# Kernel tuning notes

Hardware: AMD Instinct MI355X
Metric: run time of the kernel (lower is better)

Reference implementation:

```python
import jax, jax.numpy as jnp
import numpy as np

N, E = 4096, 131072
IN, HID, OUT = 128, 128, 256
H4, C4 = 4, HID            # first/middle GAT: 4 heads of 128 -> concat 512
CAT = H4 * C4              # 512
NH, DK = 8, OUT // 8       # dense MHA
EPS_LN = 1e-5


def setup_inputs() -> dict:
    key = jax.random.key(0)
    ks = jax.random.split(key, 32)
    s = 0.05
    inp = {
        "x": jax.random.normal(ks[0], (N, IN), jnp.float32),
        "edge_index": jax.random.randint(ks[1], (2, E), 0, N, jnp.int64),
        # GAT layer 0: in=128, heads=4, out=128
        "W0": jax.random.normal(ks[2], (IN, H4 * C4)) * s,
        "as0": jax.random.normal(ks[3], (H4, C4)) * s,
        "ad0": jax.random.normal(ks[4], (H4, C4)) * s,
        "b0": jnp.zeros((H4 * C4,)),
        # GAT layer 1: in=512, heads=4, out=128
        "W1": jax.random.normal(ks[5], (CAT, H4 * C4)) * s,
        "as1": jax.random.normal(ks[6], (H4, C4)) * s,
        "ad1": jax.random.normal(ks[7], (H4, C4)) * s,
        "b1": jnp.zeros((H4 * C4,)),
        # GAT layer 2: in=512, heads=1, out=256
        "W2": jax.random.normal(ks[8], (CAT, OUT)) * s,
        "as2": jax.random.normal(ks[9], (1, OUT)) * s,
        "ad2": jax.random.normal(ks[10], (1, OUT)) * s,
        "b2": jnp.zeros((OUT,)),
        # LayerNorms
        "g0": jnp.ones((CAT,)), "be0": jnp.zeros((CAT,)),
        "g1": jnp.ones((CAT,)), "be1": jnp.zeros((CAT,)),
        "g2": jnp.ones((OUT,)), "be2": jnp.zeros((OUT,)),
        # dense MHA on output_dim=256
        "wq": jax.random.normal(ks[11], (OUT, OUT)) * s, "bq": jnp.zeros((OUT,)),
        "wk": jax.random.normal(ks[12], (OUT, OUT)) * s, "bk": jnp.zeros((OUT,)),
        "wv": jax.random.normal(ks[13], (OUT, OUT)) * s, "bv": jnp.zeros((OUT,)),
        "wo": jax.random.normal(ks[14], (OUT, OUT)) * s, "bo": jnp.zeros((OUT,)),
    }
    return inp


def _layer_norm(x, g, b):
    mu = x.mean(-1, keepdims=True)
    var = ((x - mu) ** 2).mean(-1, keepdims=True)
    return (x - mu) * jax.lax.rsqrt(var + EPS_LN) * g + b


def _gat(x, src, dst, W, a_src, a_dst, bias, heads, out_c):
    # PyG GATConv (concat=True, negative_slope=0.2, self-loops pre-added)
    n = x.shape[0]
    xl = (x @ W).reshape(n, heads, out_c)            # [N,H,C]
    al_s = (xl * a_src).sum(-1)                      # [N,H]
    al_d = (xl * a_dst).sum(-1)                      # [N,H]
    alpha = jax.nn.leaky_relu(al_s[src] + al_d[dst], 0.2)  # [Etot,H]
    m = jax.ops.segment_max(alpha, dst, num_segments=n)
    e = jnp.exp(alpha - m[dst])
    denom = jax.ops.segment_sum(e, dst, num_segments=n)
    w = e / (denom[dst] + 1e-16)                     # [Etot,H]
    msg = w[:, :, None] * xl[src]                    # [Etot,H,C]
    out = jax.ops.segment_sum(msg, dst, num_segments=n)
    return out.reshape(n, heads * out_c) + bias


def _mha(x, wq, bq, wk, bk, wv, bv, wo, bo):
    # x: [1,N,D], 8 heads
    B, S, D = x.shape
    def split(y):
        return y.reshape(B, S, NH, DK).transpose(0, 2, 1, 3)
    Q, K, V = split(x @ wq + bq), split(x @ wk + bk), split(x @ wv + bv)
    scores = jnp.einsum('bhqd,bhkd->bhqk', Q, K) / np.sqrt(DK)
    attn = jax.nn.softmax(scores, axis=-1)
    out = jnp.einsum('bhqk,bhkd->bhqd', attn, V)
    out = out.transpose(0, 2, 1, 3).reshape(B, S, D)
    return out @ wo + bo


def reference(x, edge_index, W0, as0, ad0, b0, W1, as1, ad1, b1, W2, as2, ad2, b2,
              g0, be0, g1, be1, g2, be2, wq, bq, wk, bk, wv, bv, wo, bo):
    n = x.shape[0]
    loops = jnp.arange(n, dtype=edge_index.dtype)
    src = jnp.concatenate([edge_index[0], loops])
    dst = jnp.concatenate([edge_index[1], loops])

    # layer 0: in=128 -> 512; residual None (128 != 512)
    h = jax.nn.elu(_gat(x, src, dst, W0, as0, ad0, b0, H4, C4))
    h = _layer_norm(h, g0, be0)

    # layer 1: 512 -> 512; residual applies
    res = h
    h = jax.nn.elu(_gat(h, src, dst, W1, as1, ad1, b1, H4, C4))
    h = _layer_norm(h, g1, be1)
    h = h + res

    # layer 2: 512 -> 256, 1 head
    h = _gat(h, src, dst, W2, as2, ad2, b2, 1, OUT)
    h = _layer_norm(h, g2, be2)

    # dense self-attention over all nodes as one sequence
    h = _mha(h[None], wq, bq, wk, bk, wv, bv, wo, bo)[0]
    return h
```

## Files before the change

kernel.cpp:

```cpp
#include <hip/hip_runtime.h>
#include <math.h>

typedef __attribute__((ext_vector_type(8))) short short8;
typedef __attribute__((ext_vector_type(4))) float float4v;

#define QS 0.2550354f

#if __has_builtin(__builtin_amdgcn_exp2f)
#define EXP2(x) __builtin_amdgcn_exp2f(x)
#else
#define EXP2(x) __expf((x)*0.6931471805599453f)
#endif

__device__ __forceinline__ float waveReduceSum(float v){
  #pragma unroll
  for(int o=32;o>0;o>>=1) v += __shfl_down(v,o,64);
  return v;
}

__device__ __forceinline__ unsigned short f2bf(float f){
  unsigned int u = __float_as_uint(f);
  return (unsigned short)((u + 0x7FFFu + ((u>>16)&1u)) >> 16);
}
__device__ __forceinline__ float bf2f(unsigned short u){
  return __uint_as_float(((unsigned int)u)<<16);
}

__global__ __launch_bounds__(256) void prep(const float* __restrict__ x, unsigned short* __restrict__ xb,
                     const float* __restrict__ W0, unsigned short* __restrict__ W0t,
                     const float* __restrict__ W1, unsigned short* __restrict__ W1t,
                     const float* __restrict__ W2, unsigned short* __restrict__ W2t,
                     const float* __restrict__ wq, const float* __restrict__ wk,
                     const float* __restrict__ wv, unsigned short* __restrict__ wqkvt,
                     const float* __restrict__ bq, const float* __restrict__ bk,
                     const float* __restrict__ bv, float* __restrict__ bqkv,
                     const float* __restrict__ wo, unsigned short* __restrict__ wot,
                     const float* __restrict__ as0, const float* __restrict__ ad0, unsigned short* __restrict__ S0,
                     const float* __restrict__ as1, const float* __restrict__ ad1, unsigned short* __restrict__ S1,
                     const float* __restrict__ as2, const float* __restrict__ ad2, unsigned short* __restrict__ S2,
                     const int* __restrict__ ei, int E, int Etot, int* __restrict__ hist){
  int b = blockIdx.x, t = threadIdx.x;
  if(b < 256){
    int i = (b*256 + t)*8;
    float4 u0 = *(const float4*)(x + i);
    float4 u1 = *(const float4*)(x + i + 4);
    short8 o;
    o[0]=(short)f2bf(u0.x); o[1]=(short)f2bf(u0.y); o[2]=(short)f2bf(u0.z); o[3]=(short)f2bf(u0.w);
    o[4]=(short)f2bf(u1.x); o[5]=(short)f2bf(u1.y); o[6]=(short)f2bf(u1.z); o[7]=(short)f2bf(u1.w);
    *(short8*)(xb + i) = o;
    return;
  }
  if(b == 256){ bqkv[t] = bq[t]*QS; bqkv[256+t] = bk[t]; bqkv[512+t] = bv[t]; return; }
  if(b < 433){
    __shared__ unsigned short tile[64][65];
    int tb = b - 257;
    const float* src; unsigned short* dst; int K,N,roff,local; float sc = 1.f;
    if(tb<16){src=W0;dst=W0t;K=128;N=512;local=tb;roff=0;}
    else if(tb<80){src=W1;dst=W1t;K=512;N=512;local=tb-16;roff=0;}
    else if(tb<112){src=W2;dst=W2t;K=512;N=256;local=tb-80;roff=0;}
    else if(tb<128){src=wq;dst=wqkvt;K=256;N=256;local=tb-112;roff=0;sc=QS;}
    else if(tb<144){src=wk;dst=wqkvt;K=256;N=256;local=tb-128;roff=256;}
    else if(tb<160){src=wv;dst=wqkvt;K=256;N=256;local=tb-144;roff=512;}
    else {src=wo;dst=wot;K=256;N=256;local=tb-160;roff=0;}
    int ntiles = N>>6;
    int k0 = (local/ntiles)*64, n0 = (local%ntiles)*64;
    int r4 = t>>4, c4 = (t&15)*4;
    #pragma unroll
    for(int it=0;it<4;it++){
      int row = r4 + it*16;
      float4 v = *(const float4*)(src + (size_t)(k0+row)*N + n0 + c4);
      tile[row][c4+0]=f2bf(v.x*sc);
      tile[row][c4+1]=f2bf(v.y*sc);
      tile[row][c4+2]=f2bf(v.z*sc);
      tile[row][c4+3]=f2bf(v.w*sc);
    }
    __syncthreads();
    int r8 = t>>3, c8 = (t&7)*8;
    #pragma unroll
    for(int it=0;it<2;it++){
      int n = r8 + it*32;
      short8 o;
      #pragma unroll
      for(int j=0;j<8;j++) o[j] = (short)tile[c8+j][n];
      *(short8*)(dst + (size_t)(n0+n+roff)*K + k0 + c8) = o;
    }
    return;
  }
  if(b >= 1585){
    int e = (b-1585)*256 + t;
    if(e < Etot){
      int d = (e<E) ? (ei[E+e]&4095) : (e-E);
      atomicAdd(&hist[d], 1);
    }
    return;
  }
  int bb = b - 433;
  const float *W,*as,*ad; unsigned short* S; int K,C,H,k;
  if(bb<128){W=W0;as=as0;ad=ad0;S=S0;K=128;C=128;H=4;k=bb;}
  else if(bb<640){W=W1;as=as1;ad=ad1;S=S1;K=512;C=128;H=4;k=bb-128;}
  else {W=W2;as=as2;ad=ad2;S=S2;K=512;C=256;H=1;k=bb-640;}
  int D = H*C;
  __shared__ float s1[4], s2[4];
  int lane=t&63, wid=t>>6;
  for(int h=0;h<H;h++){
    float ps=0.f, pd=0.f;
    for(int c=t;c<C;c+=256){
      float wv2 = W[k*D + h*C + c];
      ps += wv2*as[h*C+c];
      pd += wv2*ad[h*C+c];
    }
    ps = waveReduceSum(ps); pd = waveReduceSum(pd);
    if(lane==0){ s1[wid]=ps; s2[wid]=pd; }
    __syncthreads();
    if(t==0){
      float u=s1[0]+s1[1]+s1[2]+s1[3], v=s2[0]+s2[1]+s2[2]+s2[3];
      S[h*K+k]=f2bf(u); S[(4+h)*K+k]=f2bf(v);
    }
    __syncthreads();
  }
  if(t==0){
    for(int h=H;h<4;h++){ S[h*K+k]=0; S[(4+h)*K+k]=0; }
    for(int r=8;r<16;r++) S[r*K+k]=0;
  }
}

__global__ __launch_bounds__(256) void gemm_mfma(const unsigned short* __restrict__ A,
                                                 const unsigned short* __restrict__ Bt,
                                                 const float* __restrict__ bias,
                                                 float* __restrict__ C,
                                                 unsigned short* __restrict__ Cb,
                                                 unsigned short* __restrict__ VtT,
                                                 const unsigned short* __restrict__ Wsd,
                                                 float* __restrict__ als,
                                                 float* __restrict__ ald,
                                                 int M, int K, int N){
  int t = threadIdx.x, lane = t & 63, w = t >> 6;
  int m = lane & 15, g = lane >> 4;
  int bm = blockIdx.y * 64, bn = blockIdx.x * 64;

  __shared__ unsigned short As[2][64*72];
  __shared__ unsigned short Bs[2][64*72];

  int sr = t >> 3;
  int sc = (t & 7) * 8;
  const unsigned short* Ap = A  + (bm + sr)*K + sc;
  const unsigned short* Bp = Bt + (bn + sr)*K + sc;
  bool doC = (Wsd != nullptr) && (blockIdx.x == 0);

  float4v acc[4];
  #pragma unroll
  for(int nt=0;nt<4;nt++) acc[nt] = (float4v){0.f,0.f,0.f,0.f};
  float4v acc2 = (float4v){0.f,0.f,0.f,0.f};

  short8 a0 = *(const short8*)(Ap);
  short8 a1 = *(const short8*)(Ap + 32*K);
  short8 b0 = *(const short8*)(Bp);
  short8 b1 = *(const short8*)(Bp + 32*K);

  int buf = 0;
  for(int k0=0;k0<K;k0+=64){
    *(short8*)&As[buf][sr*72 + sc]      = a0;
    *(short8*)&As[buf][(sr+32)*72 + sc] = a1;
    *(short8*)&Bs[buf][sr*72 + sc]      = b0;
    *(short8*)&Bs[buf][(sr+32)*72 + sc] = b1;
    if(k0+64 < K){
      a0 = *(const short8*)(Ap + k0+64);
      a1 = *(const short8*)(Ap + 32*K + k0+64);
      b0 = *(const short8*)(Bp + k0+64);
      b1 = *(const short8*)(Bp + 32*K + k0+64);
    }
    __syncthreads();

    #pragma unroll
    for(int ks=0;ks<2;ks++){
      short8 aA = *(const short8*)&As[buf][(w*16 + m)*72 + ks*32 + g*8];
      #pragma unroll
      for(int nt=0;nt<4;nt++){
        short8 bB = *(const short8*)&Bs[buf][(nt*16 + m)*72 + ks*32 + g*8];
        acc[nt] = __builtin_amdgcn_mfma_f32_16x16x32_bf16(aA, bB, acc[nt], 0,0,0);
      }
      if(doC){
        short8 bW = *(const short8*)(Wsd + m*K + k0 + ks*32 + g*8);
        acc2 = __builtin_amdgcn_mfma_f32_16x16x32_bf16(aA, bW, acc2, 0,0,0);
      }
    }
    buf ^= 1;
  }

  if(VtT && bn >= 512){
    __syncthreads();
    unsigned short* T = &As[0][0];
    #pragma unroll
    for(int nt=0;nt<4;nt++){
      int col = bn + nt*16 + m;
      float bv = bias ? bias[col] : 0.f;
      unsigned int r0 = __float_as_uint(acc[nt][0]+bv) + 0x8000u;
      unsigned int r1 = __float_as_uint(acc[nt][1]+bv) + 0x8000u;
      unsigned int r2 = __float_as_uint(acc[nt][2]+bv) + 0x8000u;
      unsigned int r3 = __float_as_uint(acc[nt][3]+bv) + 0x8000u;
      uint2 pk;
      pk.x = __builtin_amdgcn_perm(r1, r0, 0x07060302u);
      pk.y = __builtin_amdgcn_perm(r3, r2, 0x07060302u);
      *(uint2*)&T[(nt*16 + m)*72 + w*16 + g*4] = pk;
    }
    __syncthreads();
    int d  = t >> 2;
    int qc = (t & 3) * 16;
    short8 v0 = *(const short8*)&T[d*72 + qc];
    short8 v1 = *(const short8*)&T[d*72 + qc + 8];
    unsigned short* dst = VtT + (size_t)(bn - 512 + d)*M + bm + qc;
    *(short8*)(dst)     = v0;
    *(short8*)(dst + 8) = v1;
    return;
  }

  #pragma unroll
  for(int nt=0;nt<4;nt++){
    int col = bn + nt*16 + m;
    float bv = bias ? bias[col] : 0.f;
    #pragma unroll
    for(int r=0;r<4;r++){
      int row = bm + w*16 + g*4 + r;
      float v = acc[nt][r] + bv;
      if(C)  C[row*N + col]  = v;
      if(Cb) Cb[row*N + col] = f2bf(v);
    }
  }
  if(doC){
    #pragma unroll
    for(int r=0;r<4;r++){
      int row = bm + w*16 + g*4 + r;
      if(m<4)      als[row*4 + m]     = acc2[r];
      else if(m<8) ald[row*4 + (m-4)] = acc2[r];
    }
  }
}

__global__ __launch_bounds__(1024) void csr_scan(const int* __restrict__ hist,
                                                 int* __restrict__ row_ptr,
                                                 int* __restrict__ wcnt, int N){
  __shared__ int sh[1024];
  int t = threadIdx.x;
  int base[4];
  int s = 0;
  #pragma unroll
  for(int i=0;i<4;i++){ base[i]=s; s += hist[t*4+i]; }
  sh[t] = s;
  __syncthreads();
  for(int off=1; off<1024; off<<=1){
    int x = (t>=off) ? sh[t-off] : 0;
    __syncthreads();
    sh[t] += x;
    __syncthreads();
  }
  int excl = (t==0) ? 0 : sh[t-1];
  #pragma unroll
  for(int i=0;i<4;i++){
    row_ptr[t*4+i] = excl + base[i];
    wcnt[t*4+i]    = excl + base[i];
  }
  if(t==1023) row_ptr[N] = excl + s;
}

__global__ void csr_scatter(const int* __restrict__ ei, int E, int Etot,
                            int* __restrict__ wcnt, int* __restrict__ col){
  int e = blockIdx.x*256 + threadIdx.x;
  if(e>=Etot) return;
  int s,d;
  if(e<E){ s=ei[e]&4095; d=ei[E+e]&4095; } else { s=d=e-E; }
  int pos = atomicAdd(&wcnt[d], 1);
  col[pos] = s;
}

#define CE 128
__global__ void gat_gather_ln(const int* __restrict__ rp,
                              const int* __restrict__ col,
                              const unsigned short* __restrict__ xlb,
                              const float* __restrict__ als,
                              const float* __restrict__ ald,
                              const float* __restrict__ bias,
                              const float* __restrict__ gw,
                              const float* __restrict__ be,
                              const float* __restrict__ res,
                              float* __restrict__ out,
                              unsigned short* __restrict__ outb,
                              int D, int logC, int do_elu){
  int n = blockIdx.x, t = threadIdx.x;
  int c0 = t*2;
  int h = c0 >> logC;
  int rowW = D >> 1;
  float4 advv = *(const float4*)(ald + n*4);
  int start = rp[n], end = rp[n+1];
  const unsigned int* xw = (const unsigned int*)xlb;

  __shared__ float pw[2][CE*4];
  __shared__ int offs[2][CE];

  float acc0=0.f, acc1=0.f, den=0.f;
  int nch = (end - start + CE - 1) / CE;

  {
    int cnt = min(CE, end-start);
    if(t < cnt){
      int s = col[start+t];
      offs[0][t] = s*rowW;
      float4 av = *(const float4*)(als + s*4);
      #pragma unroll
      for(int hh=0;hh<4;hh++){
        float a = ((const float*)&av)[hh] + ((const float*)&advv)[hh];
        a = a>0.f ? a : 0.2f*a;
        pw[0][t*4+hh] = __expf(a);
      }
    }
  }

  for(int c=0;c<nch;c++){
    __syncthreads();
    if(c+1 < nch){
      int base = start + (c+1)*CE;
      int cnt = min(CE, end-base);
      int b2 = (c+1)&1;
      if(t < cnt){
        int s = col[base+t];
        offs[b2][t] = s*rowW;
        float4 av = *(const float4*)(als + s*4);
        #pragma unroll
        for(int hh=0;hh<4;hh++){
          float a = ((const float*)&av)[hh] + ((const float*)&advv)[hh];
          a = a>0.f ? a : 0.2f*a;
          pw[b2][t*4+hh] = __expf(a);
        }
      }
    }
    int base = start + c*CE;
    int cnt = min(CE, end-base);
    int b = c&1;
    #pragma unroll 8
    for(int j=0;j<cnt;j++){
      float p = pw[b][j*4+h];
      unsigned int u = xw[offs[b][j] + t];
      acc0 += p * bf2f((unsigned short)(u & 0xffffu));
      acc1 += p * bf2f((unsigned short)(u >> 16));
      den += p;
    }
  }

  float inv_d = 1.f/(den + 1e-16f);
  float v0 = acc0*inv_d + bias[c0];
  float v1 = acc1*inv_d + bias[c0+1];
  if(do_elu){
    v0 = v0>0.f ? v0 : expm1f(v0);
    v1 = v1>0.f ? v1 : expm1f(v1);
  }
  __shared__ float sh[4];
  int lane=t&63, wid=t>>6, nw = blockDim.x>>6;
  float sum = waveReduceSum(v0+v1);
  if(lane==0) sh[wid]=sum;
  __syncthreads();
  float mean = 0.f;
  for(int i=0;i<nw;i++) mean += sh[i];
  mean /= (float)D;
  __syncthreads();
  float d0 = v0-mean, d1 = v1-mean;
  float vs = waveReduceSum(d0*d0 + d1*d1);
  if(lane==0) sh[wid]=vs;
  __syncthreads();
  float var = 0.f;
  for(int i=0;i<nw;i++) var += sh[i];
  var /= (float)D;
  float inv = rsqrtf(var + 1e-5f);
  float y0 = d0*inv*gw[c0]   + be[c0];
  float y1 = d1*inv*gw[c0+1] + be[c0+1];
  if(res){ float2 rv = *(const float2*)(res + n*D + c0); y0 += rv.x; y1 += rv.y; }
  if(out) *(float2*)(out + n*D + c0) = make_float2(y0, y1);
  if(outb) ((unsigned int*)outb)[n*rowW + t] =
      (unsigned int)f2bf(y0) | ((unsigned int)f2bf(y1) << 16);
}

#define KS 4
__global__ __launch_bounds__(256) void attention12(const unsigned short* __restrict__ QKV,
                                                   const unsigned short* __restrict__ Vt,
                                                   float* __restrict__ Op,
                                                   float* __restrict__ lp, int S){
  const int RS = 768;
  int qb = blockIdx.x * 64;
  int h  = blockIdx.y;
  int ks = blockIdx.z;
  int t  = threadIdx.x;
  int lane = t & 63, w = t >> 6;
  int m = lane & 15, g = lane >> 4;
  int m7 = m & 7;

  __shared__ unsigned short Ps[64*64];
  __shared__ unsigned short Vs[32*64];
  __shared__ unsigned short Ks[64*36];

  short8 aQ = *(const short8*)(QKV + (qb + w*16 + m)*RS + h*32 + g*8);

  float4v o0 = {0.f,0.f,0.f,0.f}, o1 = {0.f,0.f,0.f,0.f};
  float den = 0.f;

  int r8 = t>>3, c8 = t&7;
  int kr = t>>2, kc = (t&3)*8;
  int kA = ks*(S/KS), kB = kA + S/KS;

  short8 v  = *(const short8*)(Vt + (h*32 + r8)*S + kA + c8*8);
  short8 kv = *(const short8*)(QKV + (kA + kr)*RS + 256 + h*32 + kc);

  for(int kt=kA; kt<kB; kt+=64){
    __syncthreads();
    *(short8*)&Vs[r8*64 + ((c8 ^ (r8&7))<<3)] = v;
    *(short8*)&Ks[kr*36 + kc] = kv;
    if(kt+64 < kB){
      v  = *(const short8*)(Vt + (h*32 + r8)*S + kt+64 + c8*8);
      kv = *(const short8*)(QKV + (kt+64 + kr)*RS + 256 + h*32 + kc);
    }
    __syncthreads();

    #pragma unroll
    for(int nt=0;nt<4;nt++){
      short8 aK = *(const short8*)&Ks[(nt*16 + m)*36 + g*8];
      float4v acc = {0.f,0.f,0.f,0.f};
      acc = __builtin_amdgcn_mfma_f32_16x16x32_bf16(aK, aQ, acc, 0,0,0);
      float p0 = EXP2(acc[0]);
      float p1 = EXP2(acc[1]);
      float p2 = EXP2(acc[2]);
      float p3 = EXP2(acc[3]);
      den += (p0+p1)+(p2+p3);
      unsigned int r0 = __float_as_uint(p0) + 0x8000u;
      unsigned int r1 = __float_as_uint(p1) + 0x8000u;
      unsigned int r2 = __float_as_uint(p2) + 0x8000u;
      unsigned int r3 = __float_as_uint(p3) + 0x8000u;
      uint2 pk;
      pk.x = __builtin_amdgcn_perm(r1, r0, 0x07060302u);
      pk.y = __builtin_amdgcn_perm(r3, r2, 0x07060302u);
      *(uint2*)&Ps[(w*16 + m)*64 + (((2*nt + (g>>1)) ^ m7)<<3) + ((g&1)<<2)] = pk;
    }

    #pragma unroll
    for(int kh=0;kh<2;kh++){
      int swz = ((kh*4 + g) ^ m7) << 3;
      short8 aP  = *(const short8*)&Ps[(w*16 + m)*64 + swz];
      short8 bV0 = *(const short8*)&Vs[m*64       + swz];
      short8 bV1 = *(const short8*)&Vs[(16+m)*64  + swz];
      o0 = __builtin_amdgcn_mfma_f32_16x16x32_bf16(aP, bV0, o0, 0,0,0);
      o1 = __builtin_amdgcn_mfma_f32_16x16x32_bf16(aP, bV1, o1, 0,0,0);
    }
  }

  den += __shfl_xor(den, 16, 64);
  den += __shfl_xor(den, 32, 64);

  float* Ob = Op + (size_t)ks*S*256;
  #pragma unroll
  for(int r=0;r<4;r++){
    int q = qb + w*16 + g*4 + r;
    Ob[q*256 + h*32 + m]      = o0[r];
    Ob[q*256 + h*32 + 16 + m] = o1[r];
  }
  if(g==0){
    int q = qb + w*16 + m;
    lp[ks*S*8 + q*8 + h] = den;
  }
}

__global__ __launch_bounds__(256) void combine(const float* __restrict__ Op,
                                               const float* __restrict__ lp,
                                               unsigned short* __restrict__ aob, int S){
  int q = blockIdx.x, t = threadIdx.x;
  int h = t >> 5;
  float o = 0.f, l = 0.f;
  #pragma unroll
  for(int s=0;s<KS;s++) o += Op[(size_t)s*S*256 + q*256 + t];
  #pragma unroll
  for(int s=0;s<KS;s++) l += lp[s*S*8 + q*8 + h];
  aob[q*256 + t] = f2bf(o / l);
}

extern "C" void kernel_launch(void* const* d_in, const int* in_sizes, int n_in,
                              void* d_out, int out_size, void* d_ws, size_t ws_size,
                              hipStream_t stream) {
  const float* x   = (const float*)d_in[0];
  const int*   ei  = (const int*)d_in[1];
  const float* W0  = (const float*)d_in[2];
  const float* as0 = (const float*)d_in[3];
  const float* ad0 = (const float*)d_in[4];
  const float* b0  = (const float*)d_in[5];
  const float* W1  = (const float*)d_in[6];
  const float* as1 = (const float*)d_in[7];
  const float* ad1 = (const float*)d_in[8];
  const float* b1  = (const float*)d_in[9];
  const float* W2  = (const float*)d_in[10];
  const float* as2 = (const float*)d_in[11];
  const float* ad2 = (const float*)d_in[12];
  const float* b2  = (const float*)d_in[13];
  const float* g0  = (const float*)d_in[14];
  const float* be0 = (const float*)d_in[15];
  const float* g1  = (const float*)d_in[16];
  const float* be1 = (const float*)d_in[17];
  const float* g2  = (const float*)d_in[18];
  const float* be2 = (const float*)d_in[19];
  const float* wq  = (const float*)d_in[20];
  const float* bq  = (const float*)d_in[21];
  const float* wk  = (const float*)d_in[22];
  const float* bk  = (const float*)d_in[23];
  const float* wv  = (const float*)d_in[24];
  const float* bv  = (const float*)d_in[25];
  const float* wo  = (const float*)d_in[26];
  const float* bo  = (const float*)d_in[27];
  float* out = (float*)d_out;

  const int N = 4096;
  const int E = in_sizes[1] / 2;
  const int Etot = E + N;

  char* p = (char*)d_ws;
  auto alloc = [&](size_t bytes){ char* r = p; p += (bytes + 255) & ~(size_t)255; return r; };

  float* h0   = (float*)alloc(N*512*4);
  float* als  = (float*)alloc(N*4*4);
  float* ald  = (float*)alloc(N*4*4);
  unsigned short* xb   = (unsigned short*)alloc(N*128*2);
  unsigned short* xlb  = (unsigned short*)alloc(N*512*2);
  unsigned short* h0b  = (unsigned short*)alloc(N*512*2);
  unsigned short* h1b  = (unsigned short*)alloc(N*512*2);
  unsigned short* h2b  = (unsigned short*)alloc(N*256*2);
  unsigned short* QKVb = (unsigned short*)alloc((size_t)N*768*2);
  unsigned short* Vt   = (unsigned short*)alloc(256*N*2);
  unsigned short* aob  = (unsigned short*)alloc(N*256*2);
  unsigned short* W0t  = (unsigned short*)alloc(512*128*2);
  unsigned short* W1t  = (unsigned short*)alloc(512*512*2);
  unsigned short* W2t  = (unsigned short*)alloc(256*512*2);
  unsigned short* wqkvt= (unsigned short*)alloc(768*256*2);
  float* bqkv = (float*)alloc(768*4);
  unsigned short* wot  = (unsigned short*)alloc(256*256*2);
  unsigned short* Wsd0 = (unsigned short*)alloc(16*128*2);
  unsigned short* Wsd1 = (unsigned short*)alloc(16*512*2);
  unsigned short* Wsd2 = (unsigned short*)alloc(16*512*2);
  float* Op = (float*)alloc((size_t)KS*N*256*4);
  float* lp = (float*)alloc((size_t)KS*N*8*4);
  int* hist = (int*)alloc(N*4);
  int* wcnt = (int*)alloc(N*4);
  int* rp   = (int*)alloc((N+2)*4);
  int* col  = (int*)alloc(Etot*4);

  hipMemsetAsync(hist, 0, N*sizeof(int), stream);
  prep<<<1585 + (Etot+255)/256, 256, 0, stream>>>(x, xb, W0, W0t, W1, W1t, W2, W2t,
                                 wq, wk, wv, wqkvt, bq, bk, bv, bqkv, wo, wot,
                                 as0, ad0, Wsd0, as1, ad1, Wsd1, as2, ad2, Wsd2,
                                 ei, E, Etot, hist);

  csr_scan<<<1, 1024, 0, stream>>>(hist, rp, wcnt, N);
  csr_scatter<<<(Etot+255)/256, 256, 0, stream>>>(ei, E, Etot, wcnt, col);

  gemm_mfma<<<dim3(8, 64), 256, 0, stream>>>(xb, W0t, nullptr, nullptr, xlb, nullptr, Wsd0, als, ald, N, 128, 512);
  gat_gather_ln<<<N, 256, 0, stream>>>(rp, col, xlb, als, ald, b0, g0, be0,
                                       nullptr, h0, h0b, 512, 7, 1);

  gemm_mfma<<<dim3(8, 64), 256, 0, stream>>>(h0b, W1t, nullptr, nullptr, xlb, nullptr, Wsd1, als, ald, N, 512, 512);
  gat_gather_ln<<<N, 256, 0, stream>>>(rp, col, xlb, als, ald, b1, g1, be1,
                                       h0, nullptr, h1b, 512, 7, 1);

  gemm_mfma<<<dim3(4, 64), 256, 0, stream>>>(h1b, W2t, nullptr, nullptr, xlb, nullptr, Wsd2, als, ald, N, 512, 256);
  gat_gather_ln<<<N, 128, 0, stream>>>(rp, col, xlb, als, ald, b2, g2, be2,
                                       nullptr, nullptr, h2b, 256, 8, 0);

  gemm_mfma<<<dim3(12, 64), 256, 0, stream>>>(h2b, wqkvt, bqkv, nullptr, QKVb, Vt, nullptr, nullptr, nullptr, N, 256, 768);
  attention12<<<dim3(N/64, 8, KS), 256, 0, stream>>>(QKVb, Vt, Op, lp, N);
  combine<<<N, 256, 0, stream>>>(Op, lp, aob, N);
  gemm_mfma<<<dim3(4, 64), 256, 0, stream>>>(aob, wot, bo, out, nullptr, nullptr, nullptr, nullptr, nullptr, N, 256, 256);
}
```

Baseline: 268.1 us.

## Fold histogram into single-block scan, fuse edge scatter with first GEMM, halve attention split

The destination-degree histogram moves out of the prep kernel into the single-block CSR scan kernel, using shared-memory atomics, which removes the memset and the global atomics. The edge scatter that builds the CSR columns now runs as extra blocks of the layer-0 GEMM launch, so both share one launch and can run concurrently. The attention key-split factor drops from 4 to 2, which cuts partial-output traffic and combine work but leaves fewer attention blocks. The risk is that the single 1024-thread block walking all edges may be slower than the parallel global histogram.

```diff
diff --git a/kernel.cpp b/kernel.cpp
--- a/kernel.cpp
+++ b/kernel.cpp
@@ -17,7 +17,6 @@
   for(int o=32;o>0;o>>=1) v += __shfl_down(v,o,64);
   return v;
 }
-
 __device__ __forceinline__ unsigned short f2bf(float f){
   unsigned int u = __float_as_uint(f);
   return (unsigned short)((u + 0x7FFFu + ((u>>16)&1u)) >> 16);
@@ -37,8 +36,7 @@
                      const float* __restrict__ wo, unsigned short* __restrict__ wot,
                      const float* __restrict__ as0, const float* __restrict__ ad0, unsigned short* __restrict__ S0,
                      const float* __restrict__ as1, const float* __restrict__ ad1, unsigned short* __restrict__ S1,
-                     const float* __restrict__ as2, const float* __restrict__ ad2, unsigned short* __restrict__ S2,
-                     const int* __restrict__ ei, int E, int Etot, int* __restrict__ hist){
+                     const float* __restrict__ as2, const float* __restrict__ ad2, unsigned short* __restrict__ S2){
   int b = blockIdx.x, t = threadIdx.x;
   if(b < 256){
     int i = (b*256 + t)*8;
@@ -86,14 +84,6 @@
     }
     return;
   }
-  if(b >= 1585){
-    int e = (b-1585)*256 + t;
-    if(e < Etot){
-      int d = (e<E) ? (ei[E+e]&4095) : (e-E);
-      atomicAdd(&hist[d], 1);
-    }
-    return;
-  }
   int bb = b - 433;
   const float *W,*as,*ad; unsigned short* S; int K,C,H,k;
   if(bb<128){W=W0;as=as0;ad=ad0;S=S0;K=128;C=128;H=4;k=bb;}
@@ -124,28 +114,55 @@
   }
 }
 
-__global__ __launch_bounds__(256) void gemm_mfma(const unsigned short* __restrict__ A,
-                                                 const unsigned short* __restrict__ Bt,
-                                                 const float* __restrict__ bias,
-                                                 float* __restrict__ C,
-                                                 unsigned short* __restrict__ Cb,
-                                                 unsigned short* __restrict__ VtT,
-                                                 const unsigned short* __restrict__ Wsd,
-                                                 float* __restrict__ als,
-                                                 float* __restrict__ ald,
-                                                 int M, int K, int N){
+__global__ __launch_bounds__(1024) void csr_scan(const int* __restrict__ ei, int E, int Etot,
+                                                 int* __restrict__ rp, int* __restrict__ wcnt){
+  __shared__ int sh[1024];
+  __shared__ int lhist[4096];
+  int t = threadIdx.x;
+  #pragma unroll
+  for(int i=0;i<4;i++) lhist[t*4+i] = 0;
+  __syncthreads();
+  for(int e=t; e<Etot; e+=1024){
+    int d = (e<E) ? (ei[E+e]&4095) : (e-E);
+    atomicAdd(&lhist[d], 1);
+  }
+  __syncthreads();
+  int base[4]; int s=0;
+  #pragma unroll
+  for(int i=0;i<4;i++){ base[i]=s; s += lhist[t*4+i]; }
+  sh[t] = s;
+  __syncthreads();
+  for(int off=1; off<1024; off<<=1){
+    int x = (t>=off) ? sh[t-off] : 0;
+    __syncthreads();
+    sh[t] += x;
+    __syncthreads();
+  }
+  int excl = (t==0) ? 0 : sh[t-1];
+  #pragma unroll
+  for(int i=0;i<4;i++){
+    int v = excl + base[i];
+    rp[t*4+i] = v; wcnt[t*4+i] = v;
+  }
+  if(t==1023) rp[4096] = excl + s;
+}
+
+__device__ __forceinline__ void gemm_body(int bx, int by,
+                          const unsigned short* __restrict__ A, const unsigned short* __restrict__ Bt,
+                          const float* __restrict__ bias, float* __restrict__ C,
+                          unsigned short* __restrict__ Cb, unsigned short* __restrict__ VtT,
+                          const unsigned short* __restrict__ Wsd, float* __restrict__ als,
+                          float* __restrict__ ald, int M, int K, int N,
+                          unsigned short* As, unsigned short* Bs){
   int t = threadIdx.x, lane = t & 63, w = t >> 6;
   int m = lane & 15, g = lane >> 4;
-  int bm = blockIdx.y * 64, bn = blockIdx.x * 64;
-
-  __shared__ unsigned short As[2][64*72];
-  __shared__ unsigned short Bs[2][64*72];
+  int bm = by * 64, bn = bx * 64;
 
   int sr = t >> 3;
   int sc = (t & 7) * 8;
-  const unsigned short* Ap = A  + (bm + sr)*K + sc;
-  const unsigned short* Bp = Bt + (bn + sr)*K + sc;
-  bool doC = (Wsd != nullptr) && (blockIdx.x == 0);
+  const unsigned short* Ap = A  + (size_t)(bm + sr)*K + sc;
+  const unsigned short* Bp = Bt + (size_t)(bn + sr)*K + sc;
+  bool doC = (Wsd != nullptr) && (bx == 0);
 
   float4v acc[4];
   #pragma unroll
@@ -159,10 +176,10 @@
 
   int buf = 0;
   for(int k0=0;k0<K;k0+=64){
-    *(short8*)&As[buf][sr*72 + sc]      = a0;
-    *(short8*)&As[buf][(sr+32)*72 + sc] = a1;
-    *(short8*)&Bs[buf][sr*72 + sc]      = b0;
-    *(short8*)&Bs[buf][(sr+32)*72 + sc] = b1;
+    *(short8*)&As[buf*4608 + sr*72 + sc]      = a0;
+    *(short8*)&As[buf*4608 + (sr+32)*72 + sc] = a1;
+    *(short8*)&Bs[buf*4608 + sr*72 + sc]      = b0;
+    *(short8*)&Bs[buf*4608 + (sr+32)*72 + sc] = b1;
     if(k0+64 < K){
       a0 = *(const short8*)(Ap + k0+64);
       a1 = *(const short8*)(Ap + 32*K + k0+64);
@@ -173,10 +190,10 @@
 
     #pragma unroll
     for(int ks=0;ks<2;ks++){
-      short8 aA = *(const short8*)&As[buf][(w*16 + m)*72 + ks*32 + g*8];
+      short8 aA = *(const short8*)&As[buf*4608 + (w*16 + m)*72 + ks*32 + g*8];
       #pragma unroll
       for(int nt=0;nt<4;nt++){
-        short8 bB = *(const short8*)&Bs[buf][(nt*16 + m)*72 + ks*32 + g*8];
+        short8 bB = *(const short8*)&Bs[buf*4608 + (nt*16 + m)*72 + ks*32 + g*8];
         acc[nt] = __builtin_amdgcn_mfma_f32_16x16x32_bf16(aA, bB, acc[nt], 0,0,0);
       }
       if(doC){
@@ -187,9 +204,9 @@
     buf ^= 1;
   }
 
-  if(VtT && bn >= 512){
-    __syncthreads();
-    unsigned short* T = &As[0][0];
+  if(VtT != nullptr && bn >= 512){
+    __syncthreads();
+    unsigned short* T = As;
     #pragma unroll
     for(int nt=0;nt<4;nt++){
       int col = bn + nt*16 + m;
@@ -222,8 +239,8 @@
     for(int r=0;r<4;r++){
       int row = bm + w*16 + g*4 + r;
       float v = acc[nt][r] + bv;
-      if(C)  C[row*N + col]  = v;
-      if(Cb) Cb[row*N + col] = f2bf(v);
+      if(C)  C[(size_t)row*N + col]  = v;
+      if(Cb) Cb[(size_t)row*N + col] = f2bf(v);
     }
   }
   if(doC){
@@ -236,40 +253,42 @@
   }
 }
 
-__global__ __launch_bounds__(1024) void csr_scan(const int* __restrict__ hist,
-                                                 int* __restrict__ row_ptr,
-                                                 int* __restrict__ wcnt, int N){
-  __shared__ int sh[1024];
-  int t = threadIdx.x;
-  int base[4];
-  int s = 0;
-  #pragma unroll
-  for(int i=0;i<4;i++){ base[i]=s; s += hist[t*4+i]; }
-  sh[t] = s;
-  __syncthreads();
-  for(int off=1; off<1024; off<<=1){
-    int x = (t>=off) ? sh[t-off] : 0;
-    __syncthreads();
-    sh[t] += x;
-    __syncthreads();
-  }
-  int excl = (t==0) ? 0 : sh[t-1];
-  #pragma unroll
-  for(int i=0;i<4;i++){
-    row_ptr[t*4+i] = excl + base[i];
-    wcnt[t*4+i]    = excl + base[i];
-  }
-  if(t==1023) row_ptr[N] = excl + s;
-}
-
-__global__ void csr_scatter(const int* __restrict__ ei, int E, int Etot,
-                            int* __restrict__ wcnt, int* __restrict__ col){
-  int e = blockIdx.x*256 + threadIdx.x;
-  if(e>=Etot) return;
-  int s,d;
-  if(e<E){ s=ei[e]&4095; d=ei[E+e]&4095; } else { s=d=e-E; }
-  int pos = atomicAdd(&wcnt[d], 1);
-  col[pos] = s;
+__global__ __launch_bounds__(256) void gemm_mfma(const unsigned short* __restrict__ A,
+                                                 const unsigned short* __restrict__ Bt,
+                                                 const float* __restrict__ bias,
+                                                 float* __restrict__ C,
+                                                 unsigned short* __restrict__ Cb,
+                                                 unsigned short* __restrict__ VtT,
+                                                 const unsigned short* __restrict__ Wsd,
+                                                 float* __restrict__ als,
+                                                 float* __restrict__ ald,
+                                                 int M, int K, int N){
+  __shared__ unsigned short As[2*4608];
+  __shared__ unsigned short Bs[2*4608];
+  gemm_body(blockIdx.x, blockIdx.y, A, Bt, bias, C, Cb, VtT, Wsd, als, ald, M, K, N, As, Bs);
+}
+
+__global__ __launch_bounds__(256) void gemm0_scatter(const unsigned short* __restrict__ A,
+                                                     const unsigned short* __restrict__ Bt,
+                                                     unsigned short* __restrict__ Cb,
+                                                     const unsigned short* __restrict__ Wsd,
+                                                     float* __restrict__ als, float* __restrict__ ald,
+                                                     const int* __restrict__ ei, int E, int Etot,
+                                                     int* __restrict__ wcnt, int* __restrict__ col){
+  __shared__ unsigned short As[2*4608];
+  __shared__ unsigned short Bs[2*4608];
+  int u = blockIdx.x;
+  if(u < 512){
+    gemm_body(u & 7, u >> 3, A, Bt, nullptr, nullptr, Cb, nullptr, Wsd, als, ald, 4096, 128, 512, As, Bs);
+  } else {
+    int e = (u-512)*256 + threadIdx.x;
+    if(e < Etot){
+      int s,d;
+      if(e < E){ s = ei[e]&4095; d = ei[E+e]&4095; } else { s = d = e - E; }
+      int pos = atomicAdd(&wcnt[d], 1);
+      col[pos] = s;
+    }
+  }
 }
 
 #define CE 128
@@ -377,7 +396,7 @@
       (unsigned int)f2bf(y0) | ((unsigned int)f2bf(y1) << 16);
 }
 
-#define KS 4
+#define KS 2
 __global__ __launch_bounds__(256) void attention12(const unsigned short* __restrict__ QKV,
                                                    const unsigned short* __restrict__ Vt,
                                                    float* __restrict__ Op,
@@ -539,21 +558,18 @@
   unsigned short* Wsd2 = (unsigned short*)alloc(16*512*2);
   float* Op = (float*)alloc((size_t)KS*N*256*4);
   float* lp = (float*)alloc((size_t)KS*N*8*4);
-  int* hist = (int*)alloc(N*4);
   int* wcnt = (int*)alloc(N*4);
   int* rp   = (int*)alloc((N+2)*4);
   int* col  = (int*)alloc(Etot*4);
 
-  hipMemsetAsync(hist, 0, N*sizeof(int), stream);
-  prep<<<1585 + (Etot+255)/256, 256, 0, stream>>>(x, xb, W0, W0t, W1, W1t, W2, W2t,
+  prep<<<1585, 256, 0, stream>>>(x, xb, W0, W0t, W1, W1t, W2, W2t,
                                  wq, wk, wv, wqkvt, bq, bk, bv, bqkv, wo, wot,
-                                 as0, ad0, Wsd0, as1, ad1, Wsd1, as2, ad2, Wsd2,
-                                 ei, E, Etot, hist);
-
-  csr_scan<<<1, 1024, 0, stream>>>(hist, rp, wcnt, N);
-  csr_scatter<<<(Etot+255)/256, 256, 0, stream>>>(ei, E, Etot, wcnt, col);
-
-  gemm_mfma<<<dim3(8, 64), 256, 0, stream>>>(xb, W0t, nullptr, nullptr, xlb, nullptr, Wsd0, als, ald, N, 128, 512);
+                                 as0, ad0, Wsd0, as1, ad1, Wsd1, as2, ad2, Wsd2);
+
+  csr_scan<<<1, 1024, 0, stream>>>(ei, E, Etot, rp, wcnt);
+
+  gemm0_scatter<<<512 + (Etot+255)/256, 256, 0, stream>>>(xb, W0t, xlb, Wsd0, als, ald,
+                                                          ei, E, Etot, wcnt, col);
   gat_gather_ln<<<N, 256, 0, stream>>>(rp, col, xlb, als, ald, b0, g0, be0,
                                        nullptr, h0, h0b, 512, 7, 1);
 
```

After: 301.6 us. 12.5% more time.
